# Performance work log

Hardware: AMD Instinct MI355X
Metric: run time of the kernel (lower is better)

Reference implementation:

```python
import jax, jax.numpy as jnp
import numpy as np

B, S = 2, 1024
V, D, H, L, F, M = 50257, 768, 12, 6, 3072, 1024
DK = D // H
EPS = 1e-5


def _layer_norm(x, g, b):
    mu = jnp.mean(x, axis=-1, keepdims=True)
    var = jnp.mean(jnp.square(x - mu), axis=-1, keepdims=True)
    return (x - mu) * jax.lax.rsqrt(var + EPS) * g + b


def setup_inputs() -> dict:
    key = jax.random.key(0)
    ks = jax.random.split(key, 20)
    std = 0.02
    inp = {
        'input_ids': jax.random.randint(ks[0], (B, S), 0, V),
        'tok_emb': jax.random.normal(ks[1], (V, D), jnp.float32) * std,
        'pos_emb': jax.random.normal(ks[2], (M, D), jnp.float32) * std,
        # per-layer stacked params; linear weights stored as [in, out] (y = x @ W)
        'wq': jax.random.normal(ks[3], (L, D, D), jnp.float32) * std,
        'wk': jax.random.normal(ks[4], (L, D, D), jnp.float32) * std,
        'wv': jax.random.normal(ks[5], (L, D, D), jnp.float32) * std,
        'wo': jax.random.normal(ks[6], (L, D, D), jnp.float32) * std,
        'bo': jnp.zeros((L, D), jnp.float32),
        'fc_w': jax.random.normal(ks[7], (L, D, F), jnp.float32) * std,
        'fc_b': jnp.zeros((L, F), jnp.float32),
        'proj_w': jax.random.normal(ks[8], (L, F, D), jnp.float32) * std,
        'proj_b': jnp.zeros((L, D), jnp.float32),
        'ln1_g': jnp.ones((L, D), jnp.float32),
        'ln1_b': jnp.zeros((L, D), jnp.float32),
        'ln2_g': jnp.ones((L, D), jnp.float32),
        'ln2_b': jnp.zeros((L, D), jnp.float32),
        'lnf_g': jnp.ones((D,), jnp.float32),
        'lnf_b': jnp.zeros((D,), jnp.float32),
        'out_w': jax.random.normal(ks[9], (D, V), jnp.float32) * std,
    }
    return inp


def reference(input_ids, tok_emb, pos_emb, wq, wk, wv, wo, bo, fc_w, fc_b,
              proj_w, proj_b, ln1_g, ln1_b, ln2_g, ln2_b, lnf_g, lnf_b, out_w):
    b, s = input_ids.shape
    x = tok_emb[input_ids] + pos_emb[jnp.arange(s)][None, :, :]  # [B,S,D]
    causal = jnp.tril(jnp.ones((s, s), bool))  # [S,S]
    scale = 1.0 / np.sqrt(DK)
    for l in range(L):
        xn = _layer_norm(x, ln1_g[l], ln1_b[l])
        q = (xn @ wq[l]).reshape(b, s, H, DK).transpose(0, 2, 1, 3)
        k = (xn @ wk[l]).reshape(b, s, H, DK).transpose(0, 2, 1, 3)
        v = (xn @ wv[l]).reshape(b, s, H, DK).transpose(0, 2, 1, 3)
        scores = jnp.einsum('bhqd,bhkd->bhqk', q, k) * scale
        scores = jnp.where(causal[None, None], scores, -1e9)
        attn = jax.nn.softmax(scores, axis=-1)
        ctx = jnp.einsum('bhqk,bhkd->bhqd', attn, v)
        ctx = ctx.transpose(0, 2, 1, 3).reshape(b, s, D)
        x = x + ctx @ wo[l] + bo[l]
        xn = _layer_norm(x, ln2_g[l], ln2_b[l])
        h = jax.nn.gelu(xn @ fc_w[l] + fc_b[l], approximate=False)
        x = x + h @ proj_w[l] + proj_b[l]
    x = _layer_norm(x, lnf_g, lnf_b)
    logits = x @ out_w  # [B,S,V]
    return logits
```

## Files before the change

### kernel.cpp

```cpp
#include <hip/hip_runtime.h>
#include <hip/hip_bf16.h>
#include <math.h>

#define BB 2
#define SS 1024
#define DD 768
#define HH 12
#define LL 6
#define FF 3072
#define VV 50257
#define DKK 64
#define NROWS (BB * SS)
#define QKVN (3 * DD)
#define QBLK 64
#define KVBLK 64

typedef __attribute__((ext_vector_type(8))) short short8v;
typedef __attribute__((ext_vector_type(4))) float f32x4;
typedef __attribute__((ext_vector_type(4))) int int4v;

__device__ __forceinline__ float gelu_f(float x) {
    return 0.5f * x * (1.0f + erff(x * 0.70710678118654752440f));
}

__global__ __launch_bounds__(256) void embed_kernel(
    const int* __restrict__ ids, const float* __restrict__ tok,
    const float* __restrict__ pos, float* __restrict__ x) {
    int row = blockIdx.x;
    int s = row & (SS - 1);
    int id = ids[row];
    const float* t = tok + (size_t)id * DD;
    const float* p = pos + (size_t)s * DD;
    float* xr = x + (size_t)row * DD;
    for (int i = threadIdx.x; i < DD; i += 256)
        xr[i] = t[i] + p[i];
}

__global__ __launch_bounds__(256) void ln_kernel(
    const float* __restrict__ x, const float* __restrict__ g,
    const float* __restrict__ b, float* __restrict__ out) {
    int row = blockIdx.x;
    int tid = threadIdx.x;
    const float* xr = x + (size_t)row * DD;
    float v0 = xr[tid], v1 = xr[tid + 256], v2 = xr[tid + 512];
    __shared__ float red[256];
    red[tid] = v0 + v1 + v2;
    __syncthreads();
    for (int s2 = 128; s2 > 0; s2 >>= 1) {
        if (tid < s2) red[tid] += red[tid + s2];
        __syncthreads();
    }
    float mu = red[0] * (1.0f / DD);
    __syncthreads();
    float d0 = v0 - mu, d1 = v1 - mu, d2 = v2 - mu;
    red[tid] = d0 * d0 + d1 * d1 + d2 * d2;
    __syncthreads();
    for (int s2 = 128; s2 > 0; s2 >>= 1) {
        if (tid < s2) red[tid] += red[tid + s2];
        __syncthreads();
    }
    float r = rsqrtf(red[0] * (1.0f / DD) + 1e-5f);
    float* o = out + (size_t)row * DD;
    o[tid]       = d0 * r * g[tid]       + b[tid];
    o[tid + 256] = d1 * r * g[tid + 256] + b[tid + 256];
    o[tid + 512] = d2 * r * g[tid + 512] + b[tid + 512];
}

__global__ __launch_bounds__(256) void ln_bf16_kernel(
    const float* __restrict__ x, const float* __restrict__ g,
    const float* __restrict__ b, __hip_bfloat16* __restrict__ out) {
    int row = blockIdx.x;
    int tid = threadIdx.x;
    const float* xr = x + (size_t)row * DD;
    float v0 = xr[tid], v1 = xr[tid + 256], v2 = xr[tid + 512];
    __shared__ float red[256];
    red[tid] = v0 + v1 + v2;
    __syncthreads();
    for (int s2 = 128; s2 > 0; s2 >>= 1) {
        if (tid < s2) red[tid] += red[tid + s2];
        __syncthreads();
    }
    float mu = red[0] * (1.0f / DD);
    __syncthreads();
    float d0 = v0 - mu, d1 = v1 - mu, d2 = v2 - mu;
    red[tid] = d0 * d0 + d1 * d1 + d2 * d2;
    __syncthreads();
    for (int s2 = 128; s2 > 0; s2 >>= 1) {
        if (tid < s2) red[tid] += red[tid + s2];
        __syncthreads();
    }
    float r = rsqrtf(red[0] * (1.0f / DD) + 1e-5f);
    __hip_bfloat16* o = out + (size_t)row * DD;
    o[tid]       = __float2bfloat16(d0 * r * g[tid]       + b[tid]);
    o[tid + 256] = __float2bfloat16(d1 * r * g[tid + 256] + b[tid + 256]);
    o[tid + 512] = __float2bfloat16(d2 * r * g[tid + 512] + b[tid + 512]);
}

__global__ __launch_bounds__(256) void transpose_cvt_kernel(
    const float* __restrict__ W, __hip_bfloat16* __restrict__ Wt, int K, int N) {
    __shared__ float t[32][33];
    int bn = blockIdx.x * 32, bk = blockIdx.y * 32;
    int tx = threadIdx.x & 31, ty = threadIdx.x >> 5;
    for (int r = ty; r < 32; r += 8)
        t[r][tx] = (bn + tx < N) ? W[(size_t)(bk + r) * N + bn + tx] : 0.0f;
    __syncthreads();
    for (int r = ty; r < 32; r += 8) {
        int n = bn + r;
        if (n < N) Wt[(size_t)n * K + bk + tx] = __float2bfloat16(t[tx][r]);
    }
}

#define LDSOFF(row, ks) (((row) * 64) + ((((ks) ^ (((row) >> 1) & 3))) << 4))
#define SWZ128(row, byteoff) \
    ((row) * 128 + (((((byteoff) >> 4) ^ ((row) & 7)) & 7) << 4) + ((byteoff) & 15))

template<int BM, int BN>
__global__ __launch_bounds__(256) void gemm_mfma_kernel(
    const __hip_bfloat16* __restrict__ A, const __hip_bfloat16* __restrict__ Wt,
    const float* __restrict__ bias, const float* __restrict__ residual,
    float* __restrict__ Cf, __hip_bfloat16* __restrict__ Cb,
    int M, int N, int K, int do_gelu) {
    constexpr int BK = 32;
    constexpr int UA = (BM * 4) / 256;
    constexpr int UB = (BN * 4) / 256;
    constexpr int FM = BM / 32;
    constexpr int FN = BN / 32;
    __shared__ __align__(16) char As[BM * 64];
    __shared__ __align__(16) char Bs[BN * 64];

    const int tid = threadIdx.x;
    const int lane = tid & 63;
    const int wid = tid >> 6;
    const int bm = blockIdx.y * BM;
    const int bn = blockIdx.x * BN;
    const int r16 = lane & 15;
    const int kg = lane >> 4;
    const int wm = (wid >> 1) * (FM * 16);
    const int wn = (wid & 1) * (FN * 16);

    f32x4 acc[FM][FN];
    const f32x4 zf = {0.0f, 0.0f, 0.0f, 0.0f};
#pragma unroll
    for (int i = 0; i < FM; ++i)
#pragma unroll
        for (int j = 0; j < FN; ++j) acc[i][j] = zf;

    int4v areg[UA], breg[UB];
    const int4v zi = {0, 0, 0, 0};

#pragma unroll
    for (int u = 0; u < UA; ++u) {
        int c = tid + u * 256, row = c >> 2, sl = c & 3;
        areg[u] = *(const int4v*)(A + (size_t)(bm + row) * K + sl * 8);
    }
#pragma unroll
    for (int u = 0; u < UB; ++u) {
        int c = tid + u * 256, row = c >> 2, sl = c & 3;
        int4v bv = zi;
        if (bn + row < N) bv = *(const int4v*)(Wt + (size_t)(bn + row) * K + sl * 8);
        breg[u] = bv;
    }

    for (int k0 = 0; k0 < K; k0 += BK) {
        __syncthreads();
#pragma unroll
        for (int u = 0; u < UA; ++u) {
            int c = tid + u * 256, row = c >> 2, sl = c & 3;
            *(int4v*)(As + LDSOFF(row, sl)) = areg[u];
        }
#pragma unroll
        for (int u = 0; u < UB; ++u) {
            int c = tid + u * 256, row = c >> 2, sl = c & 3;
            *(int4v*)(Bs + LDSOFF(row, sl)) = breg[u];
        }
        __syncthreads();
        int kn = k0 + BK;
        if (kn < K) {
#pragma unroll
            for (int u = 0; u < UA; ++u) {
                int c = tid + u * 256, row = c >> 2, sl = c & 3;
                areg[u] = *(const int4v*)(A + (size_t)(bm + row) * K + kn + sl * 8);
            }
#pragma unroll
            for (int u = 0; u < UB; ++u) {
                int c = tid + u * 256, row = c >> 2, sl = c & 3;
                int4v bv = zi;
                if (bn + row < N) bv = *(const int4v*)(Wt + (size_t)(bn + row) * K + kn + sl * 8);
                breg[u] = bv;
            }
        }
        short8v af[FM], bfr[FN];
#pragma unroll
        for (int i = 0; i < FM; ++i) {
            int row = wm + i * 16 + r16;
            af[i] = *(const short8v*)(As + LDSOFF(row, kg));
        }
#pragma unroll
        for (int j = 0; j < FN; ++j) {
            int row = wn + j * 16 + r16;
            bfr[j] = *(const short8v*)(Bs + LDSOFF(row, kg));
        }
#pragma unroll
        for (int i = 0; i < FM; ++i)
#pragma unroll
            for (int j = 0; j < FN; ++j)
                acc[i][j] = __builtin_amdgcn_mfma_f32_16x16x32_bf16(
                    af[i], bfr[j], acc[i][j], 0, 0, 0);
    }

    const int rg = lane >> 4;
#pragma unroll
    for (int i = 0; i < FM; ++i) {
#pragma unroll
        for (int j = 0; j < FN; ++j) {
            int col = bn + wn + j * 16 + r16;
            if (col < N) {
#pragma unroll
                for (int r = 0; r < 4; ++r) {
                    int row = bm + wm + i * 16 + rg * 4 + r;
                    float v = acc[i][j][r];
                    if (bias) v += bias[col];
                    if (do_gelu) v = gelu_f(v);
                    size_t o = (size_t)row * N + col;
                    if (residual) v += residual[o];
                    if (Cf) Cf[o] = v;
                    else Cb[o] = __float2bfloat16(v);
                }
            }
        }
    }
}

__global__ __launch_bounds__(256) void qkv_gemm_kernel(
    const __hip_bfloat16* __restrict__ A, const __hip_bfloat16* __restrict__ Wt,
    __hip_bfloat16* __restrict__ qh, __hip_bfloat16* __restrict__ kh,
    __hip_bfloat16* __restrict__ vt) {
    constexpr int BM = 128, BN = 128, BK = 32;
    constexpr int K = DD;
    constexpr int UA = 2, UB = 2, FM = 4, FN = 4;
    __shared__ __align__(16) char As[BM * 64];
    __shared__ __align__(16) char Bs[BN * 64];

    const int tid = threadIdx.x;
    const int lane = tid & 63;
    const int wid = tid >> 6;
    const int bm = blockIdx.y * BM;
    const int bn = blockIdx.x * BN;
    const int r16 = lane & 15;
    const int kg = lane >> 4;
    const int wm = (wid >> 1) * 64;
    const int wn = (wid & 1) * 64;

    f32x4 acc[FM][FN];
    const f32x4 zf = {0.0f, 0.0f, 0.0f, 0.0f};
#pragma unroll
    for (int i = 0; i < FM; ++i)
#pragma unroll
        for (int j = 0; j < FN; ++j) acc[i][j] = zf;

    int4v areg[UA], breg[UB];
#pragma unroll
    for (int u = 0; u < UA; ++u) {
        int c = tid + u * 256, row = c >> 2, sl = c & 3;
        areg[u] = *(const int4v*)(A + (size_t)(bm + row) * K + sl * 8);
    }
#pragma unroll
    for (int u = 0; u < UB; ++u) {
        int c = tid + u * 256, row = c >> 2, sl = c & 3;
        breg[u] = *(const int4v*)(Wt + (size_t)(bn + row) * K + sl * 8);
    }

    for (int k0 = 0; k0 < K; k0 += BK) {
        __syncthreads();
#pragma unroll
        for (int u = 0; u < UA; ++u) {
            int c = tid + u * 256, row = c >> 2, sl = c & 3;
            *(int4v*)(As + LDSOFF(row, sl)) = areg[u];
        }
#pragma unroll
        for (int u = 0; u < UB; ++u) {
            int c = tid + u * 256, row = c >> 2, sl = c & 3;
            *(int4v*)(Bs + LDSOFF(row, sl)) = breg[u];
        }
        __syncthreads();
        int kn = k0 + BK;
        if (kn < K) {
#pragma unroll
            for (int u = 0; u < UA; ++u) {
                int c = tid + u * 256, row = c >> 2, sl = c & 3;
                areg[u] = *(const int4v*)(A + (size_t)(bm + row) * K + kn + sl * 8);
            }
#pragma unroll
            for (int u = 0; u < UB; ++u) {
                int c = tid + u * 256, row = c >> 2, sl = c & 3;
                breg[u] = *(const int4v*)(Wt + (size_t)(bn + row) * K + kn + sl * 8);
            }
        }
        short8v af[FM], bfr[FN];
#pragma unroll
        for (int i = 0; i < FM; ++i)
            af[i] = *(const short8v*)(As + LDSOFF(wm + i * 16 + r16, kg));
#pragma unroll
        for (int j = 0; j < FN; ++j)
            bfr[j] = *(const short8v*)(Bs + LDSOFF(wn + j * 16 + r16, kg));
#pragma unroll
        for (int i = 0; i < FM; ++i)
#pragma unroll
            for (int j = 0; j < FN; ++j)
                acc[i][j] = __builtin_amdgcn_mfma_f32_16x16x32_bf16(
                    af[i], bfr[j], acc[i][j], 0, 0, 0);
    }

#pragma unroll
    for (int i = 0; i < FM; ++i) {
#pragma unroll
        for (int j = 0; j < FN; ++j) {
            int col = bn + wn + j * 16 + r16;
#pragma unroll
            for (int r = 0; r < 4; ++r) {
                int row = bm + wm + i * 16 + kg * 4 + r;
                int b = row >> 10, s = row & (SS - 1);
                float v = acc[i][j][r];
                if (col < DD) {
                    int h = col >> 6, d = col & 63;
                    qh[((size_t)(b * HH + h) * SS + s) * DKK + d] =
                        __float2bfloat16(v * 0.125f);
                } else if (col < 2 * DD) {
                    int c = col - DD, h = c >> 6, d = c & 63;
                    kh[((size_t)(b * HH + h) * SS + s) * DKK + d] = __float2bfloat16(v);
                } else {
                    int c = col - 2 * DD, h = c >> 6, d = c & 63;
                    vt[((size_t)(b * HH + h) * DKK + d) * SS + s] = __float2bfloat16(v);
                }
            }
        }
    }
}

__global__ __launch_bounds__(256) void flash_attn_kernel(
    const __hip_bfloat16* __restrict__ qh, const __hip_bfloat16* __restrict__ kh,
    const __hip_bfloat16* __restrict__ vt, __hip_bfloat16* __restrict__ ctx) {
    __shared__ __align__(16) char Ks[KVBLK * 128];
    __shared__ __align__(16) char Vs[DKK * 128];
    __shared__ __align__(16) char Ps[4][16 * 128];

    const int bh = blockIdx.x;
    const int qt = (gridDim.y - 1) - blockIdx.y;
    const int q0 = qt * QBLK;
    const int b = bh / HH;
    const int h = bh - b * HH;
    const int tid = threadIdx.x;
    const int lane = tid & 63;
    const int w = tid >> 6;
    const int r16 = lane & 15;
    const int kg = lane >> 4;
    char* Pw = Ps[w];

    const size_t qbase = ((size_t)bh * SS + q0 + w * 16 + r16) * DKK;
    short8v qf0 = *(const short8v*)(qh + qbase + kg * 8);
    short8v qf1 = *(const short8v*)(qh + qbase + 32 + kg * 8);

    f32x4 acc_o[4];
    const f32x4 zf = {0.0f, 0.0f, 0.0f, 0.0f};
    float m[4], l[4];
#pragma unroll
    for (int j = 0; j < 4; ++j) acc_o[j] = zf;
#pragma unroll
    for (int r = 0; r < 4; ++r) { m[r] = -1e30f; l[r] = 0.0f; }

    const int nt = qt + 1;
    for (int t = 0; t < nt; ++t) {
        __syncthreads();
        {
            const __hip_bfloat16* kp = kh + ((size_t)bh * SS + t * KVBLK) * DKK;
            const __hip_bfloat16* vp = vt + (size_t)bh * DKK * SS + t * KVBLK;
#pragma unroll
            for (int u = 0; u < 2; ++u) {
                int c = tid + u * 256;
                int row = c >> 3, slot = c & 7;
                *(int4v*)(Ks + SWZ128(row, slot * 16)) =
                    *(const int4v*)(kp + (size_t)row * DKK + slot * 8);
                *(int4v*)(Vs + SWZ128(row, slot * 16)) =
                    *(const int4v*)(vp + (size_t)row * SS + slot * 8);
            }
        }
        __syncthreads();

        f32x4 s[4];
#pragma unroll
        for (int j = 0; j < 4; ++j) s[j] = zf;
#pragma unroll
        for (int j = 0; j < 4; ++j) {
            short8v k0f = *(const short8v*)(Ks + SWZ128(j * 16 + r16, kg * 16));
            short8v k1f = *(const short8v*)(Ks + SWZ128(j * 16 + r16, 64 + kg * 16));
            s[j] = __builtin_amdgcn_mfma_f32_16x16x32_bf16(qf0, k0f, s[j], 0, 0, 0);
            s[j] = __builtin_amdgcn_mfma_f32_16x16x32_bf16(qf1, k1f, s[j], 0, 0, 0);
        }

        if (t == qt) {
#pragma unroll
            for (int j = 0; j < 4; ++j)
#pragma unroll
                for (int r = 0; r < 4; ++r)
                    if (j * 16 + r16 > w * 16 + kg * 4 + r) s[j][r] = -1e30f;
        }

        float alpha[4], rsum[4];
#pragma unroll
        for (int r = 0; r < 4; ++r) {
            float v = fmaxf(fmaxf(s[0][r], s[1][r]), fmaxf(s[2][r], s[3][r]));
#pragma unroll
            for (int d2 = 1; d2 < 16; d2 <<= 1)
                v = fmaxf(v, __shfl_xor(v, d2));
            float mnew = fmaxf(m[r], v);
            alpha[r] = __expf(m[r] - mnew);
            m[r] = mnew;
            rsum[r] = 0.0f;
        }
#pragma unroll
        for (int j = 0; j < 4; ++j)
#pragma unroll
            for (int r = 0; r < 4; ++r) {
                float p = __expf(s[j][r] - m[r]);
                rsum[r] += p;
                *(__hip_bfloat16*)(Pw + SWZ128(kg * 4 + r, (j * 16 + r16) * 2)) =
                    __float2bfloat16(p);
            }
#pragma unroll
        for (int r = 0; r < 4; ++r) {
#pragma unroll
            for (int d2 = 1; d2 < 16; d2 <<= 1)
                rsum[r] += __shfl_xor(rsum[r], d2);
            l[r] = l[r] * alpha[r] + rsum[r];
        }
#pragma unroll
        for (int j = 0; j < 4; ++j)
#pragma unroll
            for (int r = 0; r < 4; ++r) acc_o[j][r] *= alpha[r];

        short8v pa0 = *(const short8v*)(Pw + SWZ128(r16, kg * 16));
        short8v pa1 = *(const short8v*)(Pw + SWZ128(r16, 64 + kg * 16));
#pragma unroll
        for (int j = 0; j < 4; ++j) {
            short8v v0f = *(const short8v*)(Vs + SWZ128(j * 16 + r16, kg * 16));
            short8v v1f = *(const short8v*)(Vs + SWZ128(j * 16 + r16, 64 + kg * 16));
            acc_o[j] = __builtin_amdgcn_mfma_f32_16x16x32_bf16(pa0, v0f, acc_o[j], 0, 0, 0);
            acc_o[j] = __builtin_amdgcn_mfma_f32_16x16x32_bf16(pa1, v1f, acc_o[j], 0, 0, 0);
        }
    }

#pragma unroll
    for (int r = 0; r < 4; ++r) {
        float inv = 1.0f / l[r];
        int row = q0 + w * 16 + kg * 4 + r;
        __hip_bfloat16* cp = ctx + ((size_t)(b * SS) + row) * DD + h * DKK;
#pragma unroll
        for (int j = 0; j < 4; ++j)
            cp[j * 16 + r16] = __float2bfloat16(acc_o[j][r] * inv);
    }
}

__global__ __launch_bounds__(256) void gemm_kernel(
    const float* __restrict__ A, const float* __restrict__ W,
    const float* __restrict__ bias, const float* __restrict__ residual,
    float* __restrict__ C, int M, int N, int K, int do_gelu) {
    __shared__ float As[16][64];
    __shared__ float Ws[16][68];
    int tid = threadIdx.x;
    int bn = blockIdx.x * 64, bm = blockIdx.y * 64;
    int tx = tid & 15, ty = tid >> 4;
    int ar = tid >> 2, ak = (tid & 3) << 2;
    int wr = tid >> 4, wc = (tid & 15) << 2;
    bool n_vec = ((N & 3) == 0);
    float acc[4][4] = {};
    for (int k0 = 0; k0 < K; k0 += 16) {
        float4 av = *(const float4*)&A[(size_t)(bm + ar) * K + (k0 + ak)];
        As[ak + 0][ar] = av.x; As[ak + 1][ar] = av.y;
        As[ak + 2][ar] = av.z; As[ak + 3][ar] = av.w;
        int gn = bn + wc;
        const float* wp = &W[(size_t)(k0 + wr) * N + gn];
        float w0, w1, w2, w3;
        if (n_vec && gn + 3 < N) {
            float4 wv4 = *(const float4*)wp;
            w0 = wv4.x; w1 = wv4.y; w2 = wv4.z; w3 = wv4.w;
        } else {
            w0 = (gn + 0 < N) ? wp[0] : 0.0f;
            w1 = (gn + 1 < N) ? wp[1] : 0.0f;
            w2 = (gn + 2 < N) ? wp[2] : 0.0f;
            w3 = (gn + 3 < N) ? wp[3] : 0.0f;
        }
        Ws[wr][wc + 0] = w0; Ws[wr][wc + 1] = w1;
        Ws[wr][wc + 2] = w2; Ws[wr][wc + 3] = w3;
        __syncthreads();
#pragma unroll
        for (int kk = 0; kk < 16; ++kk) {
            float a[4], w[4];
#pragma unroll
            for (int i = 0; i < 4; ++i) a[i] = As[kk][ty * 4 + i];
#pragma unroll
            for (int j = 0; j < 4; ++j) w[j] = Ws[kk][tx * 4 + j];
#pragma unroll
            for (int i = 0; i < 4; ++i)
#pragma unroll
                for (int j = 0; j < 4; ++j)
                    acc[i][j] = fmaf(a[i], w[j], acc[i][j]);
        }
        __syncthreads();
    }
#pragma unroll
    for (int i = 0; i < 4; ++i) {
        int row = bm + ty * 4 + i;
#pragma unroll
        for (int j = 0; j < 4; ++j) {
            int col = bn + tx * 4 + j;
            if (col < N) {
                float val = acc[i][j];
                if (bias) val += bias[col];
                if (do_gelu) val = gelu_f(val);
                if (residual) val += residual[(size_t)row * N + col];
                C[(size_t)row * N + col] = val;
            }
        }
    }
}

__global__ __launch_bounds__(256) void attn_kernel(
    const float* __restrict__ q, const float* __restrict__ k,
    const float* __restrict__ v, float* __restrict__ ctx) {
    int bid = blockIdx.x;
    int qi = bid & (SS - 1);
    int bh = bid >> 10;
    int h = bh % HH;
    int b = bh / HH;
    int tid = threadIdx.x;
    __shared__ float qs[DKK];
    __shared__ float p[SS];
    __shared__ float red[256];
    __shared__ float ctx_red[4][DKK];
    const float* qrow = q + ((size_t)(b * SS + qi)) * DD + h * DKK;
    if (tid < DKK) qs[tid] = qrow[tid];
    __syncthreads();
    int nk = qi + 1;
    const float scale = 0.125f;
    for (int ki = tid; ki < nk; ki += 256) {
        const float* krow = k + ((size_t)(b * SS + ki)) * DD + h * DKK;
        float dot = 0.0f;
#pragma unroll
        for (int d = 0; d < DKK; d += 4) {
            float4 kv = *(const float4*)&krow[d];
            dot += qs[d] * kv.x + qs[d + 1] * kv.y + qs[d + 2] * kv.z + qs[d + 3] * kv.w;
        }
        p[ki] = dot * scale;
    }
    __syncthreads();
    float lmax = -1e30f;
    for (int ki = tid; ki < nk; ki += 256) lmax = fmaxf(lmax, p[ki]);
    red[tid] = lmax;
    __syncthreads();
    for (int s2 = 128; s2 > 0; s2 >>= 1) {
        if (tid < s2) red[tid] = fmaxf(red[tid], red[tid + s2]);
        __syncthreads();
    }
    float mm = red[0];
    __syncthreads();
    float lsum = 0.0f;
    for (int ki = tid; ki < nk; ki += 256) {
        float e = __expf(p[ki] - mm);
        p[ki] = e;
        lsum += e;
    }
    red[tid] = lsum;
    __syncthreads();
    for (int s2 = 128; s2 > 0; s2 >>= 1) {
        if (tid < s2) red[tid] += red[tid + s2];
        __syncthreads();
    }
    float inv = 1.0f / red[0];
    int d = tid & 63;
    int chunk = tid >> 6;
    float accd = 0.0f;
    for (int ki = chunk; ki < nk; ki += 4)
        accd += p[ki] * v[((size_t)(b * SS + ki)) * DD + h * DKK + d];
    ctx_red[chunk][d] = accd;
    __syncthreads();
    if (tid < DKK) {
        float sum = (ctx_red[0][tid] + ctx_red[1][tid]) + (ctx_red[2][tid] + ctx_red[3][tid]);
        ctx[((size_t)(b * SS + qi)) * DD + h * DKK + tid] = sum * inv;
    }
}

extern "C" void kernel_launch(void* const* d_in, const int* in_sizes, int n_in,
                              void* d_out, int out_size, void* d_ws, size_t ws_size,
                              hipStream_t stream) {
    const int*   ids    = (const int*)  d_in[0];
    const float* tok    = (const float*)d_in[1];
    const float* pos    = (const float*)d_in[2];
    const float* wq     = (const float*)d_in[3];
    const float* wk     = (const float*)d_in[4];
    const float* wv     = (const float*)d_in[5];
    const float* wo     = (const float*)d_in[6];
    const float* bo     = (const float*)d_in[7];
    const float* fc_w   = (const float*)d_in[8];
    const float* fc_b   = (const float*)d_in[9];
    const float* proj_w = (const float*)d_in[10];
    const float* proj_b = (const float*)d_in[11];
    const float* ln1_g  = (const float*)d_in[12];
    const float* ln1_b  = (const float*)d_in[13];
    const float* ln2_g  = (const float*)d_in[14];
    const float* ln2_b  = (const float*)d_in[15];
    const float* lnf_g  = (const float*)d_in[16];
    const float* lnf_b  = (const float*)d_in[17];
    const float* out_w  = (const float*)d_in[18];
    float* out = (float*)d_out;

    dim3 blk(256);

    const size_t SZ_X   = (size_t)NROWS * DD * 4;
    const size_t SZ_XN  = (size_t)NROWS * DD * 2;
    const size_t SZ_HD  = (size_t)BB * HH * SS * DKK * 2;
    const size_t SZ_CTX = (size_t)NROWS * DD * 2;
    const size_t SZ_H   = (size_t)NROWS * FF * 2;
    const size_t SZ_WT  = (size_t)50304 * DD * 2;
    const size_t NEED   = SZ_X + SZ_XN + 3 * SZ_HD + SZ_CTX + SZ_H + SZ_WT;

    if (ws_size >= NEED) {
        char* p = (char*)d_ws;
        float*          x    = (float*)p;          p += SZ_X;
        __hip_bfloat16* xn   = (__hip_bfloat16*)p; p += SZ_XN;
        __hip_bfloat16* qhb  = (__hip_bfloat16*)p; p += SZ_HD;
        __hip_bfloat16* khb  = (__hip_bfloat16*)p; p += SZ_HD;
        __hip_bfloat16* vtb  = (__hip_bfloat16*)p; p += SZ_HD;
        __hip_bfloat16* ctx  = (__hip_bfloat16*)p; p += SZ_CTX;
        __hip_bfloat16* hbuf = (__hip_bfloat16*)p; p += SZ_H;
        __hip_bfloat16* Wt   = (__hip_bfloat16*)p;

        dim3 tD(DD / 32, DD / 32);
        dim3 tF(FF / 32, DD / 32);
        dim3 tP(DD / 32, FF / 32);
        dim3 tV((VV + 31) / 32, DD / 32);

        dim3 gQKV(QKVN / 128, NROWS / 128);
        dim3 gFC(FF / 128, NROWS / 128);
        dim3 gWO(DD / 64, NROWS / 64);
        dim3 gV((VV + 127) / 128, NROWS / 128);
        dim3 gA(BB * HH, SS / QBLK);

        embed_kernel<<<NROWS, blk, 0, stream>>>(ids, tok, pos, x);

        for (int l = 0; l < LL; ++l) {
            const float* wq_l = wq + (size_t)l * DD * DD;
            const float* wk_l = wk + (size_t)l * DD * DD;
            const float* wv_l = wv + (size_t)l * DD * DD;
            const float* wo_l = wo + (size_t)l * DD * DD;
            const float* fc_w_l = fc_w + (size_t)l * DD * FF;
            const float* pj_w_l = proj_w + (size_t)l * FF * DD;

            ln_bf16_kernel<<<NROWS, blk, 0, stream>>>(x, ln1_g + l * DD, ln1_b + l * DD, xn);
            transpose_cvt_kernel<<<tD, blk, 0, stream>>>(wq_l, Wt, DD, DD);
            transpose_cvt_kernel<<<tD, blk, 0, stream>>>(wk_l, Wt + (size_t)DD * DD, DD, DD);
            transpose_cvt_kernel<<<tD, blk, 0, stream>>>(wv_l, Wt + (size_t)2 * DD * DD, DD, DD);
            qkv_gemm_kernel<<<gQKV, blk, 0, stream>>>(xn, Wt, qhb, khb, vtb);
            flash_attn_kernel<<<gA, blk, 0, stream>>>(qhb, khb, vtb, ctx);
            transpose_cvt_kernel<<<tD, blk, 0, stream>>>(wo_l, Wt, DD, DD);
            gemm_mfma_kernel<64, 64><<<gWO, blk, 0, stream>>>(
                ctx, Wt, bo + l * DD, x, x, nullptr, NROWS, DD, DD, 0);
            ln_bf16_kernel<<<NROWS, blk, 0, stream>>>(x, ln2_g + l * DD, ln2_b + l * DD, xn);
            transpose_cvt_kernel<<<tF, blk, 0, stream>>>(fc_w_l, Wt, DD, FF);
            gemm_mfma_kernel<128, 128><<<gFC, blk, 0, stream>>>(
                xn, Wt, fc_b + l * FF, nullptr, nullptr, hbuf, NROWS, FF, DD, 1);
            transpose_cvt_kernel<<<tP, blk, 0, stream>>>(pj_w_l, Wt, FF, DD);
            gemm_mfma_kernel<64, 64><<<gWO, blk, 0, stream>>>(
                hbuf, Wt, proj_b + l * DD, x, x, nullptr, NROWS, DD, FF, 0);
        }

        ln_bf16_kernel<<<NROWS, blk, 0, stream>>>(x, lnf_g, lnf_b, xn);
        transpose_cvt_kernel<<<tV, blk, 0, stream>>>(out_w, Wt, DD, VV);
        gemm_mfma_kernel<128, 128><<<gV, blk, 0, stream>>>(
            xn, Wt, nullptr, nullptr, out, nullptr, NROWS, VV, DD, 0);
        return;
    }

    const size_t XSZ = (size_t)NROWS * DD;
    float* ws = (float*)d_ws;
    float* x  = ws;
    float* xn = x  + XSZ;
    float* qb = xn + XSZ;
    float* kb = qb + XSZ;
    float* vb = kb + XSZ;
    float* cb = vb + XSZ;
    float* hb = cb + XSZ;

    dim3 gD((DD + 63) / 64, NROWS / 64);
    dim3 gF((FF + 63) / 64, NROWS / 64);
    dim3 gV2((VV + 63) / 64, NROWS / 64);

    embed_kernel<<<NROWS, blk, 0, stream>>>(ids, tok, pos, x);
    for (int l = 0; l < LL; ++l) {
        const float* wq_l = wq + (size_t)l * DD * DD;
        const float* wk_l = wk + (size_t)l * DD * DD;
        const float* wv_l = wv + (size_t)l * DD * DD;
        const float* wo_l = wo + (size_t)l * DD * DD;
        const float* fc_w_l = fc_w + (size_t)l * DD * FF;
        const float* pj_w_l = proj_w + (size_t)l * FF * DD;
        ln_kernel<<<NROWS, blk, 0, stream>>>(x, ln1_g + l * DD, ln1_b + l * DD, xn);
        gemm_kernel<<<gD, blk, 0, stream>>>(xn, wq_l, nullptr, nullptr, qb, NROWS, DD, DD, 0);
        gemm_kernel<<<gD, blk, 0, stream>>>(xn, wk_l, nullptr, nullptr, kb, NROWS, DD, DD, 0);
        gemm_kernel<<<gD, blk, 0, stream>>>(xn, wv_l, nullptr, nullptr, vb, NROWS, DD, DD, 0);
        attn_kernel<<<BB * HH * SS, blk, 0, stream>>>(qb, kb, vb, cb);
        gemm_kernel<<<gD, blk, 0, stream>>>(cb, wo_l, bo + l * DD, x, x, NROWS, DD, DD, 0);
        ln_kernel<<<NROWS, blk, 0, stream>>>(x, ln2_g + l * DD, ln2_b + l * DD, xn);
        gemm_kernel<<<gF, blk, 0, stream>>>(xn, fc_w_l, fc_b + l * FF, nullptr, hb, NROWS, FF, DD, 1);
        gemm_kernel<<<gD, blk, 0, stream>>>(hb, pj_w_l, proj_b + l * DD, x, x, NROWS, DD, FF, 0);
    }
    ln_kernel<<<NROWS, blk, 0, stream>>>(x, lnf_g, lnf_b, xn);
    gemm_kernel<<<gV2, blk, 0, stream>>>(xn, out_w, nullptr, nullptr, out, NROWS, VV, DD, 0);
}
```

Before: 1.573 ms.

## Batch all weight transposes into one launch and remap GEMM tiles for locality

When the workspace is large enough, all per-layer weight transposes and the output projection transpose are done in a single up-front kernel writing into a per-layer bf16 buffer. This replaces about 37 small transpose launches with one large one. GEMM kernels now use a 1D grid with a tile remap that walks M-tiles first and spreads consecutive blocks across 8 interleaved groups, likely to line up with XCDs and improve L2 reuse of weight tiles. The workspace needed grows to hold all converted weights, and the old per-layer path is kept as a fallback.

```diff
diff --git a/kernel.cpp b/kernel.cpp
--- a/kernel.cpp
+++ b/kernel.cpp
@@ -15,6 +15,12 @@
 #define QBLK 64
 #define KVBLK 64
 
+#define OFF_QKV 0
+#define OFF_WO  1769472
+#define OFF_FC  2359296
+#define OFF_PROJ 4718592
+#define PL      7077888
+
 typedef __attribute__((ext_vector_type(8))) short short8v;
 typedef __attribute__((ext_vector_type(4))) float f32x4;
 typedef __attribute__((ext_vector_type(4))) int int4v;
@@ -110,16 +116,75 @@
     }
 }
 
+__global__ __launch_bounds__(256) void transpose_all_kernel(
+    const float* __restrict__ wq, const float* __restrict__ wk,
+    const float* __restrict__ wv, const float* __restrict__ wo,
+    const float* __restrict__ fc_w, const float* __restrict__ proj_w,
+    const float* __restrict__ out_w, __hip_bfloat16* __restrict__ Wt_all) {
+    int bid = blockIdx.x;
+    const float* W;
+    __hip_bfloat16* Wt;
+    int K, N, tn, tk;
+    if (bid < 6 * 6912) {
+        int l = bid / 6912, r = bid % 6912;
+        __hip_bfloat16* base = Wt_all + (size_t)l * PL;
+        if (r < 1728) {
+            int which = r / 576, idx = r % 576;
+            W = (which == 0 ? wq : (which == 1 ? wk : wv)) + (size_t)l * DD * DD;
+            Wt = base + (size_t)which * DD * DD;
+            K = DD; N = DD; tn = idx % 24; tk = idx / 24;
+        } else if (r < 2304) {
+            int idx = r - 1728;
+            W = wo + (size_t)l * DD * DD;
+            Wt = base + OFF_WO;
+            K = DD; N = DD; tn = idx % 24; tk = idx / 24;
+        } else if (r < 4608) {
+            int idx = r - 2304;
+            W = fc_w + (size_t)l * DD * FF;
+            Wt = base + OFF_FC;
+            K = DD; N = FF; tn = idx % 96; tk = idx / 96;
+        } else {
+            int idx = r - 4608;
+            W = proj_w + (size_t)l * FF * DD;
+            Wt = base + OFF_PROJ;
+            K = FF; N = DD; tn = idx % 24; tk = idx / 24;
+        }
+    } else {
+        int idx = bid - 6 * 6912;
+        W = out_w;
+        Wt = Wt_all + (size_t)6 * PL;
+        K = DD; N = VV; tn = idx % 1571; tk = idx / 1571;
+    }
+    __shared__ float t[32][33];
+    int bn = tn * 32, bk = tk * 32;
+    int tx = threadIdx.x & 31, ty = threadIdx.x >> 5;
+    for (int r = ty; r < 32; r += 8)
+        t[r][tx] = (bn + tx < N) ? W[(size_t)(bk + r) * N + bn + tx] : 0.0f;
+    __syncthreads();
+    for (int r = ty; r < 32; r += 8) {
+        int n = bn + r;
+        if (n < N) Wt[(size_t)n * K + bk + tx] = __float2bfloat16(t[tx][r]);
+    }
+}
+
 #define LDSOFF(row, ks) (((row) * 64) + ((((ks) ^ (((row) >> 1) & 3))) << 4))
 #define SWZ128(row, byteoff) \
     ((row) * 128 + (((((byteoff) >> 4) ^ ((row) & 7)) & 7) << 4) + ((byteoff) & 15))
+
+__device__ __forceinline__ void tile_remap(int mtiles, int BM, int BN, int& bm, int& bn) {
+    const int nblk = gridDim.x;
+    int hw = blockIdx.x, j = hw;
+    if ((nblk & 7) == 0) j = (hw & 7) * (nblk >> 3) + (hw >> 3);
+    bm = (j % mtiles) * BM;
+    bn = (j / mtiles) * BN;
+}
 
 template<int BM, int BN>
 __global__ __launch_bounds__(256) void gemm_mfma_kernel(
     const __hip_bfloat16* __restrict__ A, const __hip_bfloat16* __restrict__ Wt,
     const float* __restrict__ bias, const float* __restrict__ residual,
     float* __restrict__ Cf, __hip_bfloat16* __restrict__ Cb,
-    int M, int N, int K, int do_gelu) {
+    int M, int N, int K, int do_gelu, int mtiles) {
     constexpr int BK = 32;
     constexpr int UA = (BM * 4) / 256;
     constexpr int UB = (BN * 4) / 256;
@@ -131,8 +196,8 @@
     const int tid = threadIdx.x;
     const int lane = tid & 63;
     const int wid = tid >> 6;
-    const int bm = blockIdx.y * BM;
-    const int bn = blockIdx.x * BN;
+    int bm, bn;
+    tile_remap(mtiles, BM, BN, bm, bn);
     const int r16 = lane & 15;
     const int kg = lane >> 4;
     const int wm = (wid >> 1) * (FM * 16);
@@ -244,8 +309,8 @@
     const int tid = threadIdx.x;
     const int lane = tid & 63;
     const int wid = tid >> 6;
-    const int bm = blockIdx.y * BM;
-    const int bn = blockIdx.x * BN;
+    int bm, bn;
+    tile_remap(16, BM, BN, bm, bn);
     const int r16 = lane & 15;
     const int kg = lane >> 4;
     const int wm = (wid >> 1) * 64;
@@ -615,15 +680,19 @@
 
     dim3 blk(256);
 
-    const size_t SZ_X   = (size_t)NROWS * DD * 4;
-    const size_t SZ_XN  = (size_t)NROWS * DD * 2;
-    const size_t SZ_HD  = (size_t)BB * HH * SS * DKK * 2;
-    const size_t SZ_CTX = (size_t)NROWS * DD * 2;
-    const size_t SZ_H   = (size_t)NROWS * FF * 2;
-    const size_t SZ_WT  = (size_t)50304 * DD * 2;
-    const size_t NEED   = SZ_X + SZ_XN + 3 * SZ_HD + SZ_CTX + SZ_H + SZ_WT;
-
-    if (ws_size >= NEED) {
+    const size_t SZ_X    = (size_t)NROWS * DD * 4;
+    const size_t SZ_XN   = (size_t)NROWS * DD * 2;
+    const size_t SZ_HD   = (size_t)BB * HH * SS * DKK * 2;
+    const size_t SZ_CTX  = (size_t)NROWS * DD * 2;
+    const size_t SZ_H    = (size_t)NROWS * FF * 2;
+    const size_t SZ_WT1  = (size_t)50304 * DD * 2;
+    const size_t SZ_WTA  = ((size_t)6 * PL + (size_t)50304 * DD) * 2;
+    const size_t ACT     = SZ_X + SZ_XN + 3 * SZ_HD + SZ_CTX + SZ_H;
+    const size_t NEED_MID = ACT + SZ_WT1;
+    const size_t NEED_BIG = ACT + SZ_WTA;
+
+    if (ws_size >= NEED_MID) {
+        const bool big = (ws_size >= NEED_BIG);
         char* p = (char*)d_ws;
         float*          x    = (float*)p;          p += SZ_X;
         __hip_bfloat16* xn   = (__hip_bfloat16*)p; p += SZ_XN;
@@ -639,44 +708,53 @@
         dim3 tP(DD / 32, FF / 32);
         dim3 tV((VV + 31) / 32, DD / 32);
 
-        dim3 gQKV(QKVN / 128, NROWS / 128);
-        dim3 gFC(FF / 128, NROWS / 128);
-        dim3 gWO(DD / 64, NROWS / 64);
-        dim3 gV((VV + 127) / 128, NROWS / 128);
+        const int nQKV = (QKVN / 128) * (NROWS / 128);
+        const int nFC  = (FF / 128) * (NROWS / 128);
+        const int nWO  = (DD / 64) * (NROWS / 64);
+        const int nV   = ((VV + 127) / 128) * (NROWS / 128);
         dim3 gA(BB * HH, SS / QBLK);
 
+        if (big)
+            transpose_all_kernel<<<6 * 6912 + 37704, blk, 0, stream>>>(
+                wq, wk, wv, wo, fc_w, proj_w, out_w, Wt);
+
         embed_kernel<<<NROWS, blk, 0, stream>>>(ids, tok, pos, x);
 
         for (int l = 0; l < LL; ++l) {
-            const float* wq_l = wq + (size_t)l * DD * DD;
-            const float* wk_l = wk + (size_t)l * DD * DD;
-            const float* wv_l = wv + (size_t)l * DD * DD;
-            const float* wo_l = wo + (size_t)l * DD * DD;
-            const float* fc_w_l = fc_w + (size_t)l * DD * FF;
-            const float* pj_w_l = proj_w + (size_t)l * FF * DD;
+            __hip_bfloat16* qkvWt = big ? Wt + (size_t)l * PL : Wt;
+            __hip_bfloat16* woWt  = big ? Wt + (size_t)l * PL + OFF_WO : Wt;
+            __hip_bfloat16* fcWt  = big ? Wt + (size_t)l * PL + OFF_FC : Wt;
+            __hip_bfloat16* pjWt  = big ? Wt + (size_t)l * PL + OFF_PROJ : Wt;
 
             ln_bf16_kernel<<<NROWS, blk, 0, stream>>>(x, ln1_g + l * DD, ln1_b + l * DD, xn);
-            transpose_cvt_kernel<<<tD, blk, 0, stream>>>(wq_l, Wt, DD, DD);
-            transpose_cvt_kernel<<<tD, blk, 0, stream>>>(wk_l, Wt + (size_t)DD * DD, DD, DD);
-            transpose_cvt_kernel<<<tD, blk, 0, stream>>>(wv_l, Wt + (size_t)2 * DD * DD, DD, DD);
-            qkv_gemm_kernel<<<gQKV, blk, 0, stream>>>(xn, Wt, qhb, khb, vtb);
+            if (!big) {
+                transpose_cvt_kernel<<<tD, blk, 0, stream>>>(wq + (size_t)l * DD * DD, qkvWt, DD, DD);
+                transpose_cvt_kernel<<<tD, blk, 0, stream>>>(wk + (size_t)l * DD * DD, qkvWt + (size_t)DD * DD, DD, DD);
+                transpose_cvt_kernel<<<tD, blk, 0, stream>>>(wv + (size_t)l * DD * DD, qkvWt + (size_t)2 * DD * DD, DD, DD);
+            }
+            qkv_gemm_kernel<<<nQKV, blk, 0, stream>>>(xn, qkvWt, qhb, khb, vtb);
             flash_attn_kernel<<<gA, blk, 0, stream>>>(qhb, khb, vtb, ctx);
-            transpose_cvt_kernel<<<tD, blk, 0, stream>>>(wo_l, Wt, DD, DD);
-            gemm_mfma_kernel<64, 64><<<gWO, blk, 0, stream>>>(
-                ctx, Wt, bo + l * DD, x, x, nullptr, NROWS, DD, DD, 0);
+            if (!big)
+                transpose_cvt_kernel<<<tD, blk, 0, stream>>>(wo + (size_t)l * DD * DD, woWt, DD, DD);
+            gemm_mfma_kernel<64, 64><<<nWO, blk, 0, stream>>>(
+                ctx, woWt, bo + l * DD, x, x, nullptr, NROWS, DD, DD, 0, NROWS / 64);
             ln_bf16_kernel<<<NROWS, blk, 0, stream>>>(x, ln2_g + l * DD, ln2_b + l * DD, xn);
-            transpose_cvt_kernel<<<tF, blk, 0, stream>>>(fc_w_l, Wt, DD, FF);
-            gemm_mfma_kernel<128, 128><<<gFC, blk, 0, stream>>>(
-                xn, Wt, fc_b + l * FF, nullptr, nullptr, hbuf, NROWS, FF, DD, 1);
-            transpose_cvt_kernel<<<tP, blk, 0, stream>>>(pj_w_l, Wt, FF, DD);
-            gemm_mfma_kernel<64, 64><<<gWO, blk, 0, stream>>>(
-                hbuf, Wt, proj_b + l * DD, x, x, nullptr, NROWS, DD, FF, 0);
-        }
-
+            if (!big)
+                transpose_cvt_kernel<<<tF, blk, 0, stream>>>(fc_w + (size_t)l * DD * FF, fcWt, DD, FF);
+            gemm_mfma_kernel<128, 128><<<nFC, blk, 0, stream>>>(
+                xn, fcWt, fc_b + l * FF, nullptr, nullptr, hbuf, NROWS, FF, DD, 1, NROWS / 128);
+            if (!big)
+                transpose_cvt_kernel<<<tP, blk, 0, stream>>>(proj_w + (size_t)l * FF * DD, pjWt, FF, DD);
+            gemm_mfma_kernel<64, 64><<<nWO, blk, 0, stream>>>(
+                hbuf, pjWt, proj_b + l * DD, x, x, nullptr, NROWS, DD, FF, 0, NROWS / 64);
+        }
+
+        __hip_bfloat16* outWt = big ? Wt + (size_t)6 * PL : Wt;
         ln_bf16_kernel<<<NROWS, blk, 0, stream>>>(x, lnf_g, lnf_b, xn);
-        transpose_cvt_kernel<<<tV, blk, 0, stream>>>(out_w, Wt, DD, VV);
-        gemm_mfma_kernel<128, 128><<<gV, blk, 0, stream>>>(
-            xn, Wt, nullptr, nullptr, out, nullptr, NROWS, VV, DD, 0);
+        if (!big)
+            transpose_cvt_kernel<<<tV, blk, 0, stream>>>(out_w, outWt, DD, VV);
+        gemm_mfma_kernel<128, 128><<<nV, blk, 0, stream>>>(
+            xn, outWt, nullptr, nullptr, out, nullptr, NROWS, VV, DD, 0, NROWS / 128);
         return;
     }
 
```

New measurement: 1.546 ms. No clear change (-1.7%).
